# Optimization experiments

Hardware: AMD Instinct MI355X
Metric: run time of the kernel (lower is better)

## Reference

```python
import jax, jax.numpy as jnp
import numpy as np
from jax import lax

B, LS, LT, C, H, GRID = 32, 256, 128, 768, 12, 16
KEEP_RATIO = 0.7

def _ln(x, w, b):
    mu = x.mean(-1, keepdims=True)
    var = ((x - mu) ** 2).mean(-1, keepdims=True)
    return (x - mu) / jnp.sqrt(var + 1e-5) * w + b

def _gelu(x):
    return jax.nn.gelu(x, approximate=False)

def setup_inputs() -> dict:
    key = jax.random.key(0)
    ks = jax.random.split(key, 16)
    w = lambda k, s: jax.random.normal(k, s, jnp.float32) * 0.02
    N = LT + LS
    return {
        'x': jax.random.normal(ks[0], (B, N, C), jnp.float32),
        'global_index_template': jax.random.randint(ks[1], (B, LT), 0, LT).astype(jnp.int32),
        'global_index_search': jax.random.randint(ks[2], (B, LS), 0, LS).astype(jnp.int32),
        'learn_template_mask': jax.random.uniform(ks[3], (2, B, LT // 2), jnp.float32),
        'ln1_w': jnp.ones((C,), jnp.float32), 'ln1_b': jnp.zeros((C,), jnp.float32),
        'qkv_w': w(ks[4], (C, 3 * C)),
        'proj_w': w(ks[5], (C, C)), 'proj_b': jnp.zeros((C,), jnp.float32),
        'ln2_w': jnp.ones((C,), jnp.float32), 'ln2_b': jnp.zeros((C,), jnp.float32),
        'fc1_w': w(ks[6], (C, 4 * C)), 'fc1_b': jnp.zeros((4 * C,), jnp.float32),
        'fc2_w': w(ks[7], (4 * C, C)), 'fc2_b': jnp.zeros((C,), jnp.float32),
        'd1_w': w(ks[8], (3 * C, 768)), 'd1_b': jnp.zeros((768,), jnp.float32),
        'd2_w': w(ks[9], (768, 384)), 'd2_b': jnp.zeros((384,), jnp.float32),
        'd3_w': w(ks[10], (384, 192)), 'd3_b': jnp.zeros((192,), jnp.float32),
        'd4_w': w(ks[11], (192, 1)), 'd4_b': jnp.zeros((1,), jnp.float32),
    }

def reference(x, global_index_template, global_index_search, learn_template_mask,
              ln1_w, ln1_b, qkv_w, proj_w, proj_b, ln2_w, ln2_b,
              fc1_w, fc1_b, fc2_w, fc2_b,
              d1_w, d1_b, d2_w, d2_b, d3_w, d3_b, d4_w, d4_b):
    bs = x.shape[0]
    lt = global_index_template.shape[1]
    ls = global_index_search.shape[1]
    half = lt // 2
    # --- roimax target representations ---
    init_rep = jnp.max(x[:, :half] * learn_template_mask[0][..., None], axis=1, keepdims=True)   # [B,1,C]
    dyn_rep = jnp.max(x[:, half:lt] * learn_template_mask[1][..., None], axis=1, keepdims=True)  # [B,1,C]
    feat = jnp.concatenate([x[:, -ls:],
                            jnp.broadcast_to(init_rep, (bs, ls, C)),
                            jnp.broadcast_to(dyn_rep, (bs, ls, C))], axis=-1)  # [B,ls,3C]
    h = _gelu(feat @ d1_w + d1_b)
    h = _gelu(h @ d2_w + d2_b)
    h = _gelu(h @ d3_w + d3_b)
    pred = h @ d4_w + d4_b                      # [B,ls,1]
    probs = jax.nn.sigmoid(pred)                # foreground probabilities
    # --- 3x3 region-sum conv and argmax center ---
    grid = probs.reshape(bs, 1, GRID, GRID)
    kern = jnp.ones((1, 1, 3, 3), grid.dtype)
    filt = lax.conv_general_dilated(grid, kern, (1, 1), 'SAME',
                                    dimension_numbers=('NCHW', 'OIHW', 'NCHW'))
    max_idx = jnp.argmax(filt.reshape(bs, -1), axis=1)
    cx, cy = max_idx // GRID, max_idx % GRID
    gx = jnp.arange(GRID)[None, :, None]
    gy = jnp.arange(GRID)[None, None, :]
    win = lambda r: ((jnp.abs(gx - cx[:, None, None]) <= r) &
                     (jnp.abs(gy - cy[:, None, None]) <= r)).reshape(bs, GRID * GRID)
    mask7, mask11 = win(3), win(5)
    foreground = (probs > 0.5).astype(jnp.int32)          # [B,ls,1]
    selected_fg = foreground * mask7[..., None].astype(jnp.int32)
    # --- candidate elimination: keep all tokens inside 11x11 window first, then top prob ---
    lens_keep = int(np.ceil(KEEP_RATIO * ls))
    p_out = jnp.where(mask11, jnp.inf, probs[..., 0])     # [B,ls]
    order = jnp.argsort(-p_out, axis=1)                   # stable descending
    topk_idx, non_topk = order[:, :lens_keep], order[:, lens_keep:]
    keep_index = jnp.take_along_axis(global_index_search, topk_idx, axis=1)
    removed_index = jnp.take_along_axis(global_index_search, non_topk, axis=1)
    xs = jnp.take_along_axis(x[:, lt:], topk_idx[..., None], axis=1)  # [B,lens_keep,C]
    xnew = jnp.concatenate([x[:, :lt], xs], axis=1)       # [B, lt+lens_keep, C]
    sf = jnp.take_along_axis(selected_fg, topk_idx[..., None], axis=1)[..., 0]
    decision = jax.nn.one_hot(sf, 2, dtype=x.dtype)       # scatter_(2, sf, 1)
    search_policy = jnp.concatenate([jnp.zeros((bs, lens_keep, 2), x.dtype), decision], -1)
    template_policy = jnp.zeros((bs, half, 4), x.dtype).at[:, :, 0].set(1.0)
    dynamic_policy = jnp.zeros((bs, half, 4), x.dtype).at[:, :, 1].set(1.0)
    P = jnp.concatenate([template_policy, dynamic_policy, search_policy], axis=1)
    key_bg = P[:, :, 2] > 0.5    # background search tokens -> masked as attention keys
    # --- attention ---
    n = xnew.shape[1]
    dh = C // H
    hn = _ln(xnew, ln1_w, ln1_b)
    qkv = (hn @ qkv_w).reshape(bs, n, 3, H, dh).transpose(2, 0, 3, 1, 4)
    q, k, v = qkv[0], qkv[1], qkv[2]
    scores = jnp.einsum('bhnd,bhmd->bhnm', q, k) * dh ** -0.5
    scores = jnp.where(key_bg[:, None, None, :], -1e9, scores)
    attn = jax.nn.softmax(scores, axis=-1)
    out = jnp.einsum('bhnm,bhmd->bhnd', attn, v).transpose(0, 2, 1, 3).reshape(bs, n, C)
    xnew = xnew + (out @ proj_w + proj_b)
    m = _ln(xnew, ln2_w, ln2_b)
    xout = xnew + (_gelu(m @ fc1_w + fc1_b) @ fc2_w + fc2_b)
    return (xout, keep_index, removed_index, attn)
```

## Files before the change

kernel.cpp:

```cpp
#include <hip/hip_runtime.h>
#include <hip/hip_bf16.h>
#include <math.h>

#define BB 32
#define LSN 256
#define LTN 128
#define CCH 768
#define NHH 12
#define NTOK 384
#define NKEEP 180
#define NREM 76
#define NNEW 308
#define MS 8192
#define MN 9856

typedef unsigned short u16;
typedef __attribute__((ext_vector_type(8))) short s8v;
typedef __attribute__((ext_vector_type(4))) float f4v;
typedef __attribute__((ext_vector_type(2))) float f2v;

__device__ __forceinline__ u16 f2bf(float x) {
    union { __hip_bfloat16 b; u16 u; } c; c.b = __float2bfloat16(x); return c.u;
}
__device__ __forceinline__ float bf2f(u16 u) {
    return __uint_as_float(((unsigned)u) << 16);
}
__device__ __forceinline__ void gl_lds16(const u16* g, u16* l) {
    __builtin_amdgcn_global_load_lds((const __attribute__((address_space(1))) unsigned*)g,
                                     (__attribute__((address_space(3))) unsigned*)l, 16, 0, 0);
}
__device__ __forceinline__ int xcd_swz(int lin, int nwg) {
    int q = nwg >> 3, r = nwg & 7;
    int xcd = lin & 7, idx = lin >> 3;
    return (xcd < r ? xcd * (q + 1) : r * (q + 1) + (xcd - r) * q) + idx;
}

__global__ void k_fail(float* o, float v) { o[0] = v; }

__global__ void k_reps(const float* __restrict__ x, const float* __restrict__ mask,
                       float* __restrict__ rep0, float* __restrict__ rep1) {
    int b = blockIdx.x, t = threadIdx.x;
    float m0[3] = {-INFINITY, -INFINITY, -INFINITY};
    float m1[3] = {-INFINITY, -INFINITY, -INFINITY};
    for (int i = 0; i < 64; ++i) {
        float mk0 = mask[b * 64 + i];
        float mk1 = mask[BB * 64 + b * 64 + i];
        const float* r0 = x + (size_t)(b * NTOK + i) * CCH;
        const float* r1 = x + (size_t)(b * NTOK + 64 + i) * CCH;
#pragma unroll
        for (int j = 0; j < 3; ++j) {
            m0[j] = fmaxf(m0[j], r0[t + 256 * j] * mk0);
            m1[j] = fmaxf(m1[j], r1[t + 256 * j] * mk1);
        }
    }
#pragma unroll
    for (int j = 0; j < 3; ++j) {
        rep0[b * CCH + t + 256 * j] = m0[j];
        rep1[b * CCH + t + 256 * j] = m1[j];
    }
}

__device__ __forceinline__ float gelu_np(float v) {
    float t = v / 1.4142135623730951f;
    float ef = (float)erf((double)t);
    return 0.5f * v * (1.0f + ef);
}

template<int ROWMAP>
__global__ __launch_bounds__(256) void gemm_exact(const float* __restrict__ A,
                                                  const float* __restrict__ rep0, const float* __restrict__ rep1,
                                                  const float* __restrict__ W, const float* __restrict__ bias,
                                                  float* __restrict__ out, int N, int K) {
    __shared__ float As[32 * 64];
    __shared__ float Bs[32 * 64];
    int t = threadIdx.x;
    int tx = t & 15, ty = t >> 4;
    int nbx = N >> 6;
    int nwg = nbx * gridDim.y;
    int lin = blockIdx.y * nbx + blockIdx.x;
    int T = xcd_swz(lin, nwg);
    int bxs = T % nbx, bys = T / nbx;
    int bm = bys * 64, bn = bxs * 64;
    int b = bm >> 8;
    f2v acc2[4][2] = {};

    int arow = t >> 2;
    int ak = (t & 3) * 4;
    int asw = arow ^ ((ak & 4) << 2);
    size_t aoff;
    if (ROWMAP) aoff = (size_t)(b * NTOK + LTN + ((bm + arow) & 255)) * CCH;
    else        aoff = (size_t)(bm + arow) * K;

    int bkr = t >> 4, bc = (t & 15) * 4;

#define LOADA(kg) (ROWMAP ? (((kg) < CCH) ? *(const float4*)&A[aoff + (kg)] \
                    : (((kg) < 2*CCH) ? *(const float4*)&rep0[b*CCH + (kg) - CCH] \
                                      : *(const float4*)&rep1[b*CCH + (kg) - 2*CCH])) \
                   : *(const float4*)&A[aoff + (kg)])

    int nt = K >> 5;
    float4 ra0 = LOADA(ak), ra1 = LOADA(16 + ak);
    float4 rb0 = *(const float4*)&W[(size_t)bkr * N + bn + bc];
    float4 rb1 = *(const float4*)&W[(size_t)(16 + bkr) * N + bn + bc];

    for (int tile = 0; tile < nt; ++tile) {
        __syncthreads();
        As[(ak + 0) * 64 + asw] = ra0.x; As[(ak + 1) * 64 + asw] = ra0.y;
        As[(ak + 2) * 64 + asw] = ra0.z; As[(ak + 3) * 64 + asw] = ra0.w;
        As[(16 + ak + 0) * 64 + asw] = ra1.x; As[(16 + ak + 1) * 64 + asw] = ra1.y;
        As[(16 + ak + 2) * 64 + asw] = ra1.z; As[(16 + ak + 3) * 64 + asw] = ra1.w;
        *(float4*)&Bs[t * 4] = rb0;
        *(float4*)&Bs[1024 + t * 4] = rb1;
        if (tile + 1 < nt) {
            int k0 = (tile + 1) << 5;
            ra0 = LOADA(k0 + ak); ra1 = LOADA(k0 + 16 + ak);
            rb0 = *(const float4*)&W[(size_t)(k0 + bkr) * N + bn + bc];
            rb1 = *(const float4*)&W[(size_t)(k0 + 16 + bkr) * N + bn + bc];
        }
        __syncthreads();
#pragma unroll
        for (int k = 0; k < 32; ++k) {
            float a[4], bv[4];
            *(float4*)&a[0]  = *(const float4*)&As[k * 64 + ((ty * 4) ^ ((k & 4) << 2))];
            *(float4*)&bv[0] = *(const float4*)&Bs[k * 64 + tx * 4];
            f2v b0 = {bv[0], bv[1]}, b1 = {bv[2], bv[3]};
#pragma unroll
            for (int i = 0; i < 4; ++i) {
                f2v av = {a[i], a[i]};
                acc2[i][0] = __builtin_elementwise_fma(av, b0, acc2[i][0]);
                acc2[i][1] = __builtin_elementwise_fma(av, b1, acc2[i][1]);
            }
        }
    }
#undef LOADA
#pragma unroll
    for (int i = 0; i < 4; ++i) {
        int m = bm + ty * 4 + i;
        float4 o;
        o.x = gelu_np(acc2[i][0][0] + bias[bn + tx * 4 + 0]);
        o.y = gelu_np(acc2[i][0][1] + bias[bn + tx * 4 + 1]);
        o.z = gelu_np(acc2[i][1][0] + bias[bn + tx * 4 + 2]);
        o.w = gelu_np(acc2[i][1][1] + bias[bn + tx * 4 + 3]);
        *(float4*)&out[(size_t)m * N + bn + tx * 4] = o;
    }
}

__global__ void k_d4sort(const float* __restrict__ h3, const float* __restrict__ w4,
                         const float* __restrict__ b4, const int* __restrict__ gis,
                         float* __restrict__ keep_out, float* __restrict__ rem_out,
                         int* __restrict__ topk, int* __restrict__ keybg) {
    int b = blockIdx.x, t = threadIdx.x;
    __shared__ float pr[256];
    __shared__ double ft[256];
    __shared__ int cxy[2];
    __shared__ float pout[256];
    __shared__ int sf[256];
    __shared__ int ord[256];
    {
        int m = b * 256 + t;
        float acc = 0.f;
        for (int k = 0; k < 192; ++k) acc = fmaf(h3[(size_t)m * 192 + k], w4[k], acc);
        float pred = acc + b4[0];
        float ef = (float)exp(-(double)pred);
        pr[t] = 1.0f / (1.0f + ef);
    }
    __syncthreads();
    int X = t >> 4, Y = t & 15;
    double s = 0.0;
    for (int dx = -1; dx <= 1; ++dx)
        for (int dy = -1; dy <= 1; ++dy) {
            int xx = X + dx, yy = Y + dy;
            if (xx >= 0 && xx < 16 && yy >= 0 && yy < 16) s += (double)pr[xx * 16 + yy];
        }
    ft[t] = s;
    __syncthreads();
    if (t == 0) {
        double best = ft[0]; int bi = 0;
        for (int i = 1; i < 256; ++i) if (ft[i] > best) { best = ft[i]; bi = i; }
        cxy[0] = bi >> 4; cxy[1] = bi & 15;
    }
    __syncthreads();
    int cx = cxy[0], cy = cxy[1];
    int ax = X - cx; if (ax < 0) ax = -ax;
    int ay = Y - cy; if (ay < 0) ay = -ay;
    bool m7  = (ax <= 3) && (ay <= 3);
    bool m11 = (ax <= 5) && (ay <= 5);
    int fg = (pr[t] > 0.5f) ? 1 : 0;
    sf[t] = m7 ? fg : 0;
    pout[t] = m11 ? INFINITY : pr[t];
    __syncthreads();
    float pi = pout[t];
    int rank = 0;
    for (int j = 0; j < 256; ++j) {
        float pj = pout[j];
        rank += (pj > pi) || (pj == pi && j < t);
    }
    ord[rank] = t;
    __syncthreads();
    int idx = ord[t];
    int g = gis[b * 256 + idx];
    if (t < NKEEP) {
        keep_out[b * NKEEP + t] = (float)g;
        topk[b * NKEEP + t] = idx;
        keybg[b * NNEW + LTN + t] = (sf[idx] == 0) ? 1 : 0;
    } else {
        rem_out[b * NREM + (t - NKEEP)] = (float)g;
    }
    if (t < LTN) keybg[b * NNEW + t] = 0;
}

__global__ void k_xnew_ln(const float* __restrict__ x, const int* __restrict__ topk,
                          const float* __restrict__ w, const float* __restrict__ b,
                          float* __restrict__ out_x, u16* __restrict__ hn) {
    int row = blockIdx.x, t = threadIdx.x;
    int bb = row / NNEW, r = row - bb * NNEW;
    int src = (r < LTN) ? r : (LTN + topk[bb * NKEEP + (r - LTN)]);
    const float* p = x + (size_t)(bb * NTOK + src) * CCH;
    __shared__ float s1[256], s2[256];
    float v[3]; float a0 = 0.f, a1 = 0.f;
#pragma unroll
    for (int i = 0; i < 3; ++i) { v[i] = p[t + 256 * i]; a0 += v[i]; a1 += v[i] * v[i]; }
#pragma unroll
    for (int i = 0; i < 3; ++i) out_x[(size_t)row * CCH + t + 256 * i] = v[i];
    s1[t] = a0; s2[t] = a1;
    __syncthreads();
    for (int off = 128; off > 0; off >>= 1) {
        if (t < off) { s1[t] += s1[t + off]; s2[t] += s2[t + off]; }
        __syncthreads();
    }
    float mu = s1[0] * (1.0f / CCH);
    float var = s2[0] * (1.0f / CCH) - mu * mu;
    float rstd = rsqrtf(var + 1e-5f);
#pragma unroll
    for (int i = 0; i < 3; ++i) {
        int c = t + 256 * i;
        hn[(size_t)row * CCH + c] = f2bf((v[i] - mu) * rstd * w[c] + b[c]);
    }
}


__global__ void k_ln_bf(const float* __restrict__ in, const float* __restrict__ w, const float* __restrict__ b,
                        u16* __restrict__ out) {
    int row = blockIdx.x, t = threadIdx.x;
    __shared__ float s1[256], s2[256];
    const float* p = in + (size_t)row * CCH;
    float v[3]; float a0 = 0.f, a1 = 0.f;
#pragma unroll
    for (int i = 0; i < 3; ++i) { v[i] = p[t + 256 * i]; a0 += v[i]; a1 += v[i] * v[i]; }
    s1[t] = a0; s2[t] = a1;
    __syncthreads();
    for (int off = 128; off > 0; off >>= 1) {
        if (t < off) { s1[t] += s1[t + off]; s2[t] += s2[t + off]; }
        __syncthreads();
    }
    float mu = s1[0] * (1.0f / CCH);
    float var = s2[0] * (1.0f / CCH) - mu * mu;
    float rstd = rsqrtf(var + 1e-5f);
#pragma unroll
    for (int i = 0; i < 3; ++i) {
        int c = t + 256 * i;
        out[(size_t)row * CCH + c] = f2bf((v[i] - mu) * rstd * w[c] + b[c]);
    }
}

__global__ void k_prep(const float* __restrict__ qkvw, const float* __restrict__ projw,
                       const float* __restrict__ fc1w, const float* __restrict__ fc2w,
                       u16* __restrict__ qkvwT, u16* __restrict__ projwT,
                       u16* __restrict__ fc1wT, u16* __restrict__ fc2wT) {
    int id = blockIdx.x;
    int t = threadIdx.x;
    const float* W; u16* Wt; int K, N, tile;
    if (id < 1728)      { W = qkvw;  Wt = qkvwT;  K = 768;  N = 2304; tile = id; }
    else if (id < 2304) { W = projw; Wt = projwT; K = 768;  N = 768;  tile = id - 1728; }
    else if (id < 4608) { W = fc1w;  Wt = fc1wT;  K = 768;  N = 3072; tile = id - 2304; }
    else                { W = fc2w;  Wt = fc2wT;  K = 3072; N = 768;  tile = id - 4608; }
    int kt = K >> 5;
    int k0 = (tile % kt) * 32, n0 = (tile / kt) * 32;
    __shared__ float tilebuf[32][33];
    int tx = t & 31, ty = t >> 5;
    for (int i = ty; i < 32; i += 8) tilebuf[i][tx] = W[(size_t)(k0 + i) * N + n0 + tx];
    __syncthreads();
    for (int i = ty; i < 32; i += 8) Wt[(size_t)(n0 + i) * K + k0 + tx] = f2bf(tilebuf[tx][i]);
}

template<int MODE>
__global__ __launch_bounds__(256) void gemm_bf16(const u16* __restrict__ A, const u16* __restrict__ Bt,
                                                 const float* __restrict__ bias, const float* __restrict__ res,
                                                 float* __restrict__ outf, u16* __restrict__ outb,
                                                 u16* __restrict__ vbuf, int N, int K) {
    __shared__ u16 sm[2][2][4096];
    int t = threadIdx.x, lane = t & 63, wid = t >> 6;
    int nwg = gridDim.x * gridDim.y;
    int lin = blockIdx.y * gridDim.x + blockIdx.x;
    int T = xcd_swz(lin, nwg);
    int bx = T % gridDim.x, by = T / gridDim.x;
    int bm = by * 128, bn = bx * 128;
    const u16* pA[2]; const u16* pB[2];
#pragma unroll
    for (int i = 0; i < 2; ++i) {
        int L = wid * 128 + i * 64 + lane;
        int line = L >> 3, sp = L & 7, sl = sp ^ (line & 7);
        int r = (line << 1) | (sl >> 2), k0 = (sl & 3) << 3;
        pA[i] = A + (size_t)(bm + r) * K + k0;
        pB[i] = Bt + (size_t)(bn + r) * K + k0;
    }
    int wr = wid >> 1, wc = wid & 1;
    int l15 = lane & 15, l4 = lane >> 4;
    int rA = wr * 64 + l15, rB = wc * 64 + l15;
    int offA = (rA >> 1) * 128 + (((((rA & 1) << 2) | l4)) ^ ((rA >> 1) & 7)) * 16;
    int offB = (rB >> 1) * 128 + (((((rB & 1) << 2) | l4)) ^ ((rB >> 1) & 7)) * 16;
    f4v zero = {0.f, 0.f, 0.f, 0.f};
    f4v acc[4][4];
#pragma unroll
    for (int i = 0; i < 4; ++i)
#pragma unroll
        for (int j = 0; j < 4; ++j) acc[i][j] = zero;

#define STAGE_G(buf, kt) { \
    u16* da = &sm[buf][0][wid * 1024]; u16* db = &sm[buf][1][wid * 1024]; \
    gl_lds16(pA[0] + (kt) * 32, da); \
    gl_lds16(pA[1] + (kt) * 32, da + 512); \
    gl_lds16(pB[0] + (kt) * 32, db); \
    gl_lds16(pB[1] + (kt) * 32, db + 512); \
}
    int nk = K >> 5;
    STAGE_G(0, 0);
    __syncthreads();
    for (int kt = 0; kt < nk; ++kt) {
        int cur = kt & 1;
        if (kt + 1 < nk) STAGE_G(cur ^ 1, kt + 1);
        const char* bA = (const char*)&sm[cur][0][0];
        const char* bBp = (const char*)&sm[cur][1][0];
        s8v a[4], b[4];
#pragma unroll
        for (int i = 0; i < 4; ++i) {
            a[i] = *(const s8v*)(bA + offA + i * 1024);
            b[i] = *(const s8v*)(bBp + offB + i * 1024);
        }
#pragma unroll
        for (int mf = 0; mf < 4; ++mf)
#pragma unroll
            for (int nf = 0; nf < 4; ++nf)
                acc[mf][nf] = __builtin_amdgcn_mfma_f32_16x16x32_bf16(a[mf], b[nf], acc[mf][nf], 0, 0, 0);
        __syncthreads();
    }
#undef STAGE_G
#pragma unroll
    for (int mf = 0; mf < 4; ++mf)
#pragma unroll
        for (int nf = 0; nf < 4; ++nf)
#pragma unroll
            for (int j = 0; j < 4; ++j) {
                int row = bm + wr * 64 + mf * 16 + l4 * 4 + j;
                int col = bn + wc * 64 + nf * 16 + l15;
                float v = acc[mf][nf][j];
                if (MODE == 0) {
                    if (col < 1536) {
                        if (col < 768) v *= 0.125f;
                        outb[(size_t)row * 1536 + col] = f2bf(v);
                    } else {
                        vbuf[(size_t)row * 768 + (col - 1536)] = f2bf(v);
                    }
                } else if (MODE == 1) {
                    outf[(size_t)row * N + col] = v + bias[col] + res[(size_t)row * N + col];
                } else {
                    float g = v + bias[col];
                    g = 0.5f * g * (1.0f + erff(g * 0.70710678f));
                    outb[(size_t)row * N + col] = f2bf(g);
                }
            }
}

__global__ __launch_bounds__(256) void k_attn2(const u16* __restrict__ qkvQK, const u16* __restrict__ vbuf,
                                               const int* __restrict__ keybg,
                                               float* __restrict__ attn_out, u16* __restrict__ ctx) {
    __shared__ __align__(16) char smem[98560];
    u16* Qs = (u16*)smem;
    u16* Ks = (u16*)(smem + 9216);
    u16* Ss = (u16*)(smem + 55296);
    int* kb = (int*)(smem + 97280);
    float* OT = (float*)Ss;
    u16* Vts = Ks;

    int nwg = gridDim.x * gridDim.y;
    int lin = blockIdx.y * gridDim.x + blockIdx.x;
    int T = xcd_swz(lin, nwg);
    int bh = T / 5;
    int q0 = (T - bh * 5) * 64;
    int b = bh / NHH, h = bh % NHH;
    int nq = NNEW - q0; if (nq > 64) nq = 64;
    int t = threadIdx.x, lane = t & 63, wid = t >> 6;
    int l15 = lane & 15, l4 = lane >> 4;
    s8v z = {0, 0, 0, 0, 0, 0, 0, 0};

    {
        int r = t >> 2, c = (t & 3) * 16;
        u16* dst = Qs + r * 72 + c;
        if (r < nq) {
            const u16* src = qkvQK + (size_t)(b * NNEW + q0 + r) * 1536 + h * 64 + c;
            *(s8v*)dst = *(const s8v*)src;
            *(s8v*)(dst + 8) = *(const s8v*)(src + 8);
        } else { *(s8v*)dst = z; *(s8v*)(dst + 8) = z; }
    }
    for (int it = 0; it < 5; ++it) {
        int r = it * 64 + (t >> 2), c = (t & 3) * 16;
        u16* dst = Ks + r * 72 + c;
        if (r < NNEW) {
            const u16* src = qkvQK + (size_t)(b * NNEW + r) * 1536 + 768 + h * 64 + c;
            *(s8v*)dst = *(const s8v*)src;
            *(s8v*)(dst + 8) = *(const s8v*)(src + 8);
        } else { *(s8v*)dst = z; *(s8v*)(dst + 8) = z; }
    }
    for (int i = t; i < 320; i += 256) kb[i] = (i < NNEW) ? keybg[b * NNEW + i] : 1;
    __syncthreads();

    f4v zero = {0.f, 0.f, 0.f, 0.f};
    f4v acc[4][5];
#pragma unroll
    for (int i = 0; i < 4; ++i)
#pragma unroll
        for (int j = 0; j < 5; ++j) acc[i][j] = zero;
#pragma unroll
    for (int ks = 0; ks < 2; ++ks) {
        s8v a[4], bf[5];
#pragma unroll
        for (int mf = 0; mf < 4; ++mf) a[mf] = *(const s8v*)(Qs + (mf * 16 + l15) * 72 + ks * 32 + l4 * 8);
#pragma unroll
        for (int nf = 0; nf < 5; ++nf) bf[nf] = *(const s8v*)(Ks + (wid * 80 + nf * 16 + l15) * 72 + ks * 32 + l4 * 8);
#pragma unroll
        for (int mf = 0; mf < 4; ++mf)
#pragma unroll
            for (int nf = 0; nf < 5; ++nf)
                acc[mf][nf] = __builtin_amdgcn_mfma_f32_16x16x32_bf16(a[mf], bf[nf], acc[mf][nf], 0, 0, 0);
    }
#pragma unroll
    for (int nf = 0; nf < 5; ++nf) {
        int n = wid * 80 + nf * 16 + l15;
        int msk = kb[n];
#pragma unroll
        for (int mf = 0; mf < 4; ++mf)
#pragma unroll
            for (int j = 0; j < 4; ++j) {
                int q = mf * 16 + l4 * 4 + j;
                float v = msk ? -1e9f : acc[mf][nf][j];
                Ss[q * 328 + n] = f2bf(v);
            }
    }
    __syncthreads();

    {
        for (int it = 0; it < 5; ++it) {
            int tok = it * 64 + (t >> 2);
            int d0 = (t & 3) * 16;
            if (tok < NNEW) {
                const u16* src = vbuf + (size_t)(b * NNEW + tok) * 768 + h * 64 + d0;
                s8v v0 = *(const s8v*)src;
                s8v v1 = *(const s8v*)(src + 8);
#pragma unroll
                for (int j = 0; j < 8; ++j) Vts[(d0 + j) * 328 + tok] = (u16)v0[j];
#pragma unroll
                for (int j = 0; j < 8; ++j) Vts[(d0 + 8 + j) * 328 + tok] = (u16)v1[j];
            } else if (tok < 320) {
#pragma unroll
                for (int j = 0; j < 16; ++j) Vts[(d0 + j) * 328 + tok] = 0;
            }
        }
    }
    {
        int q = t >> 2, j4 = t & 3;
        u16* row = Ss + q * 328 + j4 * 80;
        float mx = -3e38f;
#pragma unroll
        for (int i = 0; i < 10; ++i) {
            s8v vv = *(const s8v*)(row + i * 8);
#pragma unroll
            for (int e = 0; e < 8; ++e) mx = fmaxf(mx, bf2f((u16)vv[e]));
        }
        mx = fmaxf(mx, __shfl_xor(mx, 1));
        mx = fmaxf(mx, __shfl_xor(mx, 2));
        float sum = 0.f;
#pragma unroll
        for (int i = 0; i < 10; ++i) {
            s8v vv = *(const s8v*)(row + i * 8);
            s8v ov;
#pragma unroll
            for (int e = 0; e < 8; ++e) {
                float ex = expf(bf2f((u16)vv[e]) - mx);
                sum += ex;
                ov[e] = (short)f2bf(ex);
            }
            *(s8v*)(row + i * 8) = ov;
        }
        sum += __shfl_xor(sum, 1);
        sum += __shfl_xor(sum, 2);
        float inv = 1.0f / sum;
#pragma unroll
        for (int i = 0; i < 10; ++i) {
            s8v vv = *(const s8v*)(row + i * 8);
            s8v ov;
            float pf[8];
#pragma unroll
            for (int e = 0; e < 8; ++e) {
                float p = bf2f((u16)vv[e]) * inv;
                pf[e] = p;
                ov[e] = (short)f2bf(p);
            }
            *(s8v*)(row + i * 8) = ov;
            if (q < nq) {
                int n0 = j4 * 80 + i * 8;
                float* dst = attn_out + ((size_t)bh * NNEW + q0 + q) * NNEW + n0;
#pragma unroll
                for (int e = 0; e < 8; ++e) if (n0 + e < NNEW) dst[e] = pf[e];
            }
        }
    }
    __syncthreads();

    f4v o[4];
#pragma unroll
    for (int i = 0; i < 4; ++i) o[i] = zero;
    int dblk = wid * 16;
#pragma unroll
    for (int ks = 0; ks < 10; ++ks) {
        s8v av = *(const s8v*)(Vts + (dblk + l15) * 328 + ks * 32 + l4 * 8);
#pragma unroll
        for (int nf = 0; nf < 4; ++nf) {
            s8v pv = *(const s8v*)(Ss + (nf * 16 + l15) * 328 + ks * 32 + l4 * 8);
            o[nf] = __builtin_amdgcn_mfma_f32_16x16x32_bf16(av, pv, o[nf], 0, 0, 0);
        }
    }
    __syncthreads();
#pragma unroll
    for (int nf = 0; nf < 4; ++nf)
#pragma unroll
        for (int j = 0; j < 4; ++j)
            OT[(dblk + l4 * 4 + j) * 65 + nf * 16 + l15] = o[nf][j];
    __syncthreads();
    {
        int q = t >> 2, c = t & 3;
        if (q < nq) {
            u16 buf[16];
#pragma unroll
            for (int i = 0; i < 16; ++i) buf[i] = f2bf(OT[(c * 16 + i) * 65 + q]);
            u16* dst = ctx + (size_t)(b * NNEW + q0 + q) * CCH + h * 64 + c * 16;
            *(s8v*)dst = *(const s8v*)&buf[0];
            *(s8v*)(dst + 8) = *(const s8v*)&buf[8];
        }
    }
}

extern "C" void kernel_launch(void* const* d_in, const int* in_sizes, int n_in,
                              void* d_out, int out_size, void* d_ws, size_t ws_size,
                              hipStream_t stream) {
    const float* x     = (const float*)d_in[0];
    const int*   gis   = (const int*)d_in[2];
    const float* mask  = (const float*)d_in[3];
    const float* ln1w  = (const float*)d_in[4];
    const float* ln1b  = (const float*)d_in[5];
    const float* qkvw  = (const float*)d_in[6];
    const float* projw = (const float*)d_in[7];
    const float* projb = (const float*)d_in[8];
    const float* ln2w  = (const float*)d_in[9];
    const float* ln2b  = (const float*)d_in[10];
    const float* fc1w  = (const float*)d_in[11];
    const float* fc1b  = (const float*)d_in[12];
    const float* fc2w  = (const float*)d_in[13];
    const float* fc2b  = (const float*)d_in[14];
    const float* d1w   = (const float*)d_in[15];
    const float* d1b   = (const float*)d_in[16];
    const float* d2w   = (const float*)d_in[17];
    const float* d2b   = (const float*)d_in[18];
    const float* d3w   = (const float*)d_in[19];
    const float* d3b   = (const float*)d_in[20];
    const float* d4w   = (const float*)d_in[21];
    const float* d4b   = (const float*)d_in[22];

    float* out_x    = (float*)d_out;
    float* out_keep = out_x + 7569408;
    float* out_rem  = out_keep + 5760;
    float* out_attn = out_rem + 2432;

    char* ws = (char*)d_ws;
    u16* hn_bf  = (u16*)(ws);
    u16* qkvQK  = (u16*)(ws + 15138816);
    u16* vbuf   = (u16*)(ws + 45416448);
    u16* fc1_bf = (u16*)(ws);
    u16* ctx_bf = (u16*)(ws + 60751872);
    u16* qkvwT  = (u16*)(ws + 75890688);
    u16* projwT = (u16*)(ws + 79429632);
    u16* fc1wT  = (u16*)(ws + 80609280);
    u16* fc2wT  = (u16*)(ws + 85327872);
    char* misc  = ws + 90046464;
    float* rep0  = (float*)(misc + 0 * 262144);
    float* rep1  = (float*)(misc + 1 * 262144);
    int*   topk  = (int*)(misc + 5 * 262144);
    int*   keybg = (int*)(misc + 6 * 262144);
    size_t required = 90046464ull + 7ull * 262144ull;
    if (ws_size < required) {
        k_fail<<<1, 1, 0, stream>>>((float*)d_out, (float)(ws_size / 1048576.0));
        return;
    }

    float* h1 = (float*)out_attn;
    float* h2 = h1 + 8192 * 768;
    float* h3 = h2 + 8192 * 384;

    k_prep<<<6912, 256, 0, stream>>>(qkvw, projw, fc1w, fc2w, qkvwT, projwT, fc1wT, fc2wT);

    k_reps<<<BB, 256, 0, stream>>>(x, mask, rep0, rep1);
    gemm_exact<1><<<dim3(12, 128), 256, 0, stream>>>(x, rep0, rep1, d1w, d1b, h1, 768, 2304);
    gemm_exact<0><<<dim3(6, 128), 256, 0, stream>>>(h1, nullptr, nullptr, d2w, d2b, h2, 384, 768);
    gemm_exact<0><<<dim3(3, 128), 256, 0, stream>>>(h2, nullptr, nullptr, d3w, d3b, h3, 192, 384);
    k_d4sort<<<BB, 256, 0, stream>>>(h3, d4w, d4b, gis, out_keep, out_rem, topk, keybg);
    k_xnew_ln<<<MN, 256, 0, stream>>>(x, topk, ln1w, ln1b, out_x, hn_bf);

    gemm_bf16<0><<<dim3(18, 77), 256, 0, stream>>>(hn_bf, qkvwT, nullptr, nullptr, nullptr, qkvQK, vbuf, 2304, 768);
    k_attn2<<<dim3(5, 384), 256, 0, stream>>>(qkvQK, vbuf, keybg, out_attn, ctx_bf);
    gemm_bf16<1><<<dim3(6, 77), 256, 0, stream>>>(ctx_bf, projwT, projb, out_x, out_x, nullptr, nullptr, 768, 768);
    k_ln_bf<<<MN, 256, 0, stream>>>(out_x, ln2w, ln2b, ctx_bf);
    gemm_bf16<2><<<dim3(24, 77), 256, 0, stream>>>(ctx_bf, fc1wT, fc1b, nullptr, nullptr, fc1_bf, nullptr, 3072, 768);
    gemm_bf16<1><<<dim3(6, 77), 256, 0, stream>>>(fc1_bf, fc2wT, fc2b, out_x, out_x, nullptr, nullptr, 768, 3072);
}
```

Measured before the change: 991.1 us.

## Fuse d1 GEMM with weight prep, smaller d3 tiles, vectorize LayerNorms, MFMA priority

The weight transpose/convert kernel is merged into the d1 GEMM launch as extra blocks, so the memory-bound prep runs alongside the compute-bound GEMM and one launch is removed. The d3 GEMM switches to 32-row tiles to double its block count for better occupancy. Both LayerNorm kernels now use float4 loads and stores with 192 active threads. s_setprio is raised around the MFMA loops in attention. The merged kernel shares one LDS size and register budget across both roles, which may limit occupancy.

```diff
diff --git a/kernel.cpp b/kernel.cpp
--- a/kernel.cpp
+++ b/kernel.cpp
@@ -18,6 +18,7 @@
 typedef __attribute__((ext_vector_type(8))) short s8v;
 typedef __attribute__((ext_vector_type(4))) float f4v;
 typedef __attribute__((ext_vector_type(2))) float f2v;
+typedef __attribute__((ext_vector_type(4))) unsigned short u4v;
 
 __device__ __forceinline__ u16 f2bf(float x) {
     union { __hip_bfloat16 b; u16 u; } c; c.b = __float2bfloat16(x); return c.u;
@@ -64,6 +65,109 @@
     float t = v / 1.4142135623730951f;
     float ef = (float)erf((double)t);
     return 0.5f * v * (1.0f + ef);
+}
+
+__device__ __forceinline__ void d1_body(const float* __restrict__ A,
+                                        const float* __restrict__ rep0, const float* __restrict__ rep1,
+                                        const float* __restrict__ W, const float* __restrict__ bias,
+                                        float* __restrict__ out, float* As, float* Bs, int lin) {
+    const int N = 768, K = 2304;
+    int t = threadIdx.x;
+    int tx = t & 15, ty = t >> 4;
+    int T = xcd_swz(lin, 1536);
+    int bxs = T % 12, bys = T / 12;
+    int bm = bys * 64, bn = bxs * 64;
+    int b = bm >> 8;
+    f2v acc2[4][2] = {};
+
+    int arow = t >> 2;
+    int ak = (t & 3) * 4;
+    int asw = arow ^ ((ak & 4) << 2);
+    size_t aoff = (size_t)(b * NTOK + LTN + ((bm + arow) & 255)) * CCH;
+
+    int bkr = t >> 4, bc = (t & 15) * 4;
+
+#define LOADA1(kg) ((((kg) < CCH) ? *(const float4*)&A[aoff + (kg)] \
+                    : (((kg) < 2*CCH) ? *(const float4*)&rep0[b*CCH + (kg) - CCH] \
+                                      : *(const float4*)&rep1[b*CCH + (kg) - 2*CCH])))
+    int nt = K >> 5;
+    float4 ra0 = LOADA1(ak), ra1 = LOADA1(16 + ak);
+    float4 rb0 = *(const float4*)&W[(size_t)bkr * N + bn + bc];
+    float4 rb1 = *(const float4*)&W[(size_t)(16 + bkr) * N + bn + bc];
+
+    for (int tile = 0; tile < nt; ++tile) {
+        __syncthreads();
+        As[(ak + 0) * 64 + asw] = ra0.x; As[(ak + 1) * 64 + asw] = ra0.y;
+        As[(ak + 2) * 64 + asw] = ra0.z; As[(ak + 3) * 64 + asw] = ra0.w;
+        As[(16 + ak + 0) * 64 + asw] = ra1.x; As[(16 + ak + 1) * 64 + asw] = ra1.y;
+        As[(16 + ak + 2) * 64 + asw] = ra1.z; As[(16 + ak + 3) * 64 + asw] = ra1.w;
+        *(float4*)&Bs[t * 4] = rb0;
+        *(float4*)&Bs[1024 + t * 4] = rb1;
+        if (tile + 1 < nt) {
+            int k0 = (tile + 1) << 5;
+            ra0 = LOADA1(k0 + ak); ra1 = LOADA1(k0 + 16 + ak);
+            rb0 = *(const float4*)&W[(size_t)(k0 + bkr) * N + bn + bc];
+            rb1 = *(const float4*)&W[(size_t)(k0 + 16 + bkr) * N + bn + bc];
+        }
+        __syncthreads();
+#pragma unroll
+        for (int k = 0; k < 32; ++k) {
+            float a[4], bv[4];
+            *(float4*)&a[0]  = *(const float4*)&As[k * 64 + ((ty * 4) ^ ((k & 4) << 2))];
+            *(float4*)&bv[0] = *(const float4*)&Bs[k * 64 + tx * 4];
+            f2v b0 = {bv[0], bv[1]}, b1 = {bv[2], bv[3]};
+#pragma unroll
+            for (int i = 0; i < 4; ++i) {
+                f2v av = {a[i], a[i]};
+                acc2[i][0] = __builtin_elementwise_fma(av, b0, acc2[i][0]);
+                acc2[i][1] = __builtin_elementwise_fma(av, b1, acc2[i][1]);
+            }
+        }
+    }
+#undef LOADA1
+#pragma unroll
+    for (int i = 0; i < 4; ++i) {
+        int m = bm + ty * 4 + i;
+        float4 o;
+        o.x = gelu_np(acc2[i][0][0] + bias[bn + tx * 4 + 0]);
+        o.y = gelu_np(acc2[i][0][1] + bias[bn + tx * 4 + 1]);
+        o.z = gelu_np(acc2[i][1][0] + bias[bn + tx * 4 + 2]);
+        o.w = gelu_np(acc2[i][1][1] + bias[bn + tx * 4 + 3]);
+        *(float4*)&out[(size_t)m * N + bn + tx * 4] = o;
+    }
+}
+
+__device__ __forceinline__ void prep_body(const float* __restrict__ qkvw, const float* __restrict__ projw,
+                                          const float* __restrict__ fc1w, const float* __restrict__ fc2w,
+                                          u16* __restrict__ qkvwT, u16* __restrict__ projwT,
+                                          u16* __restrict__ fc1wT, u16* __restrict__ fc2wT,
+                                          float* tilebuf, int id) {
+    int t = threadIdx.x;
+    const float* W; u16* Wt; int K, N, tile;
+    if (id < 1728)      { W = qkvw;  Wt = qkvwT;  K = 768;  N = 2304; tile = id; }
+    else if (id < 2304) { W = projw; Wt = projwT; K = 768;  N = 768;  tile = id - 1728; }
+    else if (id < 4608) { W = fc1w;  Wt = fc1wT;  K = 768;  N = 3072; tile = id - 2304; }
+    else                { W = fc2w;  Wt = fc2wT;  K = 3072; N = 768;  tile = id - 4608; }
+    int kt = K >> 5;
+    int k0 = (tile % kt) * 32, n0 = (tile / kt) * 32;
+    int tx = t & 31, ty = t >> 5;
+    for (int i = ty; i < 32; i += 8) tilebuf[i * 33 + tx] = W[(size_t)(k0 + i) * N + n0 + tx];
+    __syncthreads();
+    for (int i = ty; i < 32; i += 8) Wt[(size_t)(n0 + i) * K + k0 + tx] = f2bf(tilebuf[tx * 33 + i]);
+}
+
+__global__ __launch_bounds__(256) void k_d1prep(const float* __restrict__ x,
+                                                const float* __restrict__ rep0, const float* __restrict__ rep1,
+                                                const float* __restrict__ d1w, const float* __restrict__ d1b,
+                                                float* __restrict__ h1,
+                                                const float* __restrict__ qkvw, const float* __restrict__ projw,
+                                                const float* __restrict__ fc1w, const float* __restrict__ fc2w,
+                                                u16* __restrict__ qkvwT, u16* __restrict__ projwT,
+                                                u16* __restrict__ fc1wT, u16* __restrict__ fc2wT) {
+    __shared__ __align__(16) float smem[4096];
+    int id = blockIdx.x;
+    if (id < 1536) d1_body(x, rep0, rep1, d1w, d1b, h1, smem, smem + 2048, id);
+    else           prep_body(qkvw, projw, fc1w, fc2w, qkvwT, projwT, fc1wT, fc2wT, smem, id - 1536);
 }
 
 template<int ROWMAP>
@@ -136,6 +240,70 @@
 #pragma unroll
     for (int i = 0; i < 4; ++i) {
         int m = bm + ty * 4 + i;
+        float4 o;
+        o.x = gelu_np(acc2[i][0][0] + bias[bn + tx * 4 + 0]);
+        o.y = gelu_np(acc2[i][0][1] + bias[bn + tx * 4 + 1]);
+        o.z = gelu_np(acc2[i][1][0] + bias[bn + tx * 4 + 2]);
+        o.w = gelu_np(acc2[i][1][1] + bias[bn + tx * 4 + 3]);
+        *(float4*)&out[(size_t)m * N + bn + tx * 4] = o;
+    }
+}
+
+__global__ __launch_bounds__(256) void gemm_exact32(const float* __restrict__ A,
+                                                    const float* __restrict__ W, const float* __restrict__ bias,
+                                                    float* __restrict__ out, int N, int K) {
+    __shared__ float As[32 * 33];
+    __shared__ float Bs[32 * 64];
+    int t = threadIdx.x;
+    int tx = t & 15, ty = t >> 4;
+    int nbx = N >> 6;
+    int nwg = nbx * gridDim.y;
+    int lin = blockIdx.y * nbx + blockIdx.x;
+    int T = xcd_swz(lin, nwg);
+    int bxs = T % nbx, bys = T / nbx;
+    int bm = bys * 32, bn = bxs * 64;
+    f2v acc2[2][2] = {};
+
+    int arow = t >> 3;
+    int ak = (t & 7) * 4;
+    size_t aoff = (size_t)(bm + arow) * K;
+    int bkr = t >> 4, bc = (t & 15) * 4;
+
+    int nt = K >> 5;
+    float4 ra = *(const float4*)&A[aoff + ak];
+    float4 rb0 = *(const float4*)&W[(size_t)bkr * N + bn + bc];
+    float4 rb1 = *(const float4*)&W[(size_t)(16 + bkr) * N + bn + bc];
+
+    for (int tile = 0; tile < nt; ++tile) {
+        __syncthreads();
+        As[(ak + 0) * 33 + arow] = ra.x; As[(ak + 1) * 33 + arow] = ra.y;
+        As[(ak + 2) * 33 + arow] = ra.z; As[(ak + 3) * 33 + arow] = ra.w;
+        *(float4*)&Bs[t * 4] = rb0;
+        *(float4*)&Bs[1024 + t * 4] = rb1;
+        if (tile + 1 < nt) {
+            int k0 = (tile + 1) << 5;
+            ra = *(const float4*)&A[aoff + k0 + ak];
+            rb0 = *(const float4*)&W[(size_t)(k0 + bkr) * N + bn + bc];
+            rb1 = *(const float4*)&W[(size_t)(k0 + 16 + bkr) * N + bn + bc];
+        }
+        __syncthreads();
+#pragma unroll
+        for (int k = 0; k < 32; ++k) {
+            float a0 = As[k * 33 + ty * 2];
+            float a1 = As[k * 33 + ty * 2 + 1];
+            float bv[4];
+            *(float4*)&bv[0] = *(const float4*)&Bs[k * 64 + tx * 4];
+            f2v b0 = {bv[0], bv[1]}, b1 = {bv[2], bv[3]};
+            f2v av0 = {a0, a0}, av1 = {a1, a1};
+            acc2[0][0] = __builtin_elementwise_fma(av0, b0, acc2[0][0]);
+            acc2[0][1] = __builtin_elementwise_fma(av0, b1, acc2[0][1]);
+            acc2[1][0] = __builtin_elementwise_fma(av1, b0, acc2[1][0]);
+            acc2[1][1] = __builtin_elementwise_fma(av1, b1, acc2[1][1]);
+        }
+    }
+#pragma unroll
+    for (int i = 0; i < 2; ++i) {
+        int m = bm + ty * 2 + i;
         float4 o;
         o.x = gelu_np(acc2[i][0][0] + bias[bn + tx * 4 + 0]);
         o.y = gelu_np(acc2[i][0][1] + bias[bn + tx * 4 + 1]);
@@ -217,11 +385,14 @@
     int src = (r < LTN) ? r : (LTN + topk[bb * NKEEP + (r - LTN)]);
     const float* p = x + (size_t)(bb * NTOK + src) * CCH;
     __shared__ float s1[256], s2[256];
-    float v[3]; float a0 = 0.f, a1 = 0.f;
-#pragma unroll
-    for (int i = 0; i < 3; ++i) { v[i] = p[t + 256 * i]; a0 += v[i]; a1 += v[i] * v[i]; }
-#pragma unroll
-    for (int i = 0; i < 3; ++i) out_x[(size_t)row * CCH + t + 256 * i] = v[i];
+    float4 v = {0.f, 0.f, 0.f, 0.f};
+    float a0 = 0.f, a1 = 0.f;
+    if (t < 192) {
+        v = *(const float4*)&p[t * 4];
+        a0 = v.x + v.y + v.z + v.w;
+        a1 = v.x * v.x + v.y * v.y + v.z * v.z + v.w * v.w;
+        *(float4*)&out_x[(size_t)row * CCH + t * 4] = v;
+    }
     s1[t] = a0; s2[t] = a1;
     __syncthreads();
     for (int off = 128; off > 0; off >>= 1) {
@@ -231,22 +402,30 @@
     float mu = s1[0] * (1.0f / CCH);
     float var = s2[0] * (1.0f / CCH) - mu * mu;
     float rstd = rsqrtf(var + 1e-5f);
-#pragma unroll
-    for (int i = 0; i < 3; ++i) {
-        int c = t + 256 * i;
-        hn[(size_t)row * CCH + c] = f2bf((v[i] - mu) * rstd * w[c] + b[c]);
-    }
-}
-
+    if (t < 192) {
+        float4 wv = *(const float4*)&w[t * 4];
+        float4 bv = *(const float4*)&b[t * 4];
+        u4v o;
+        o[0] = f2bf((v.x - mu) * rstd * wv.x + bv.x);
+        o[1] = f2bf((v.y - mu) * rstd * wv.y + bv.y);
+        o[2] = f2bf((v.z - mu) * rstd * wv.z + bv.z);
+        o[3] = f2bf((v.w - mu) * rstd * wv.w + bv.w);
+        *(u4v*)&hn[(size_t)row * CCH + t * 4] = o;
+    }
+}
 
 __global__ void k_ln_bf(const float* __restrict__ in, const float* __restrict__ w, const float* __restrict__ b,
                         u16* __restrict__ out) {
     int row = blockIdx.x, t = threadIdx.x;
     __shared__ float s1[256], s2[256];
     const float* p = in + (size_t)row * CCH;
-    float v[3]; float a0 = 0.f, a1 = 0.f;
-#pragma unroll
-    for (int i = 0; i < 3; ++i) { v[i] = p[t + 256 * i]; a0 += v[i]; a1 += v[i] * v[i]; }
+    float4 v = {0.f, 0.f, 0.f, 0.f};
+    float a0 = 0.f, a1 = 0.f;
+    if (t < 192) {
+        v = *(const float4*)&p[t * 4];
+        a0 = v.x + v.y + v.z + v.w;
+        a1 = v.x * v.x + v.y * v.y + v.z * v.z + v.w * v.w;
+    }
     s1[t] = a0; s2[t] = a1;
     __syncthreads();
     for (int off = 128; off > 0; off >>= 1) {
@@ -256,31 +435,16 @@
     float mu = s1[0] * (1.0f / CCH);
     float var = s2[0] * (1.0f / CCH) - mu * mu;
     float rstd = rsqrtf(var + 1e-5f);
-#pragma unroll
-    for (int i = 0; i < 3; ++i) {
-        int c = t + 256 * i;
-        out[(size_t)row * CCH + c] = f2bf((v[i] - mu) * rstd * w[c] + b[c]);
-    }
-}
-
-__global__ void k_prep(const float* __restrict__ qkvw, const float* __restrict__ projw,
-                       const float* __restrict__ fc1w, const float* __restrict__ fc2w,
-                       u16* __restrict__ qkvwT, u16* __restrict__ projwT,
-                       u16* __restrict__ fc1wT, u16* __restrict__ fc2wT) {
-    int id = blockIdx.x;
-    int t = threadIdx.x;
-    const float* W; u16* Wt; int K, N, tile;
-    if (id < 1728)      { W = qkvw;  Wt = qkvwT;  K = 768;  N = 2304; tile = id; }
-    else if (id < 2304) { W = projw; Wt = projwT; K = 768;  N = 768;  tile = id - 1728; }
-    else if (id < 4608) { W = fc1w;  Wt = fc1wT;  K = 768;  N = 3072; tile = id - 2304; }
-    else                { W = fc2w;  Wt = fc2wT;  K = 3072; N = 768;  tile = id - 4608; }
-    int kt = K >> 5;
-    int k0 = (tile % kt) * 32, n0 = (tile / kt) * 32;
-    __shared__ float tilebuf[32][33];
-    int tx = t & 31, ty = t >> 5;
-    for (int i = ty; i < 32; i += 8) tilebuf[i][tx] = W[(size_t)(k0 + i) * N + n0 + tx];
-    __syncthreads();
-    for (int i = ty; i < 32; i += 8) Wt[(size_t)(n0 + i) * K + k0 + tx] = f2bf(tilebuf[tx][i]);
+    if (t < 192) {
+        float4 wv = *(const float4*)&w[t * 4];
+        float4 bv = *(const float4*)&b[t * 4];
+        u4v o;
+        o[0] = f2bf((v.x - mu) * rstd * wv.x + bv.x);
+        o[1] = f2bf((v.y - mu) * rstd * wv.y + bv.y);
+        o[2] = f2bf((v.z - mu) * rstd * wv.z + bv.z);
+        o[3] = f2bf((v.w - mu) * rstd * wv.w + bv.w);
+        *(u4v*)&out[(size_t)row * CCH + t * 4] = o;
+    }
 }
 
 template<int MODE>
@@ -420,6 +584,7 @@
     for (int i = 0; i < 4; ++i)
 #pragma unroll
         for (int j = 0; j < 5; ++j) acc[i][j] = zero;
+    __builtin_amdgcn_s_setprio(1);
 #pragma unroll
     for (int ks = 0; ks < 2; ++ks) {
         s8v a[4], bf[5];
@@ -433,6 +598,7 @@
             for (int nf = 0; nf < 5; ++nf)
                 acc[mf][nf] = __builtin_amdgcn_mfma_f32_16x16x32_bf16(a[mf], bf[nf], acc[mf][nf], 0, 0, 0);
     }
+    __builtin_amdgcn_s_setprio(0);
 #pragma unroll
     for (int nf = 0; nf < 5; ++nf) {
         int n = wid * 80 + nf * 16 + l15;
@@ -520,6 +686,7 @@
 #pragma unroll
     for (int i = 0; i < 4; ++i) o[i] = zero;
     int dblk = wid * 16;
+    __builtin_amdgcn_s_setprio(1);
 #pragma unroll
     for (int ks = 0; ks < 10; ++ks) {
         s8v av = *(const s8v*)(Vts + (dblk + l15) * 328 + ks * 32 + l4 * 8);
@@ -529,6 +696,7 @@
             o[nf] = __builtin_amdgcn_mfma_f32_16x16x32_bf16(av, pv, o[nf], 0, 0, 0);
         }
     }
+    __builtin_amdgcn_s_setprio(0);
     __syncthreads();
 #pragma unroll
     for (int nf = 0; nf < 4; ++nf)
@@ -605,12 +773,11 @@
     float* h2 = h1 + 8192 * 768;
     float* h3 = h2 + 8192 * 384;
 
-    k_prep<<<6912, 256, 0, stream>>>(qkvw, projw, fc1w, fc2w, qkvwT, projwT, fc1wT, fc2wT);
-
     k_reps<<<BB, 256, 0, stream>>>(x, mask, rep0, rep1);
-    gemm_exact<1><<<dim3(12, 128), 256, 0, stream>>>(x, rep0, rep1, d1w, d1b, h1, 768, 2304);
+    k_d1prep<<<8448, 256, 0, stream>>>(x, rep0, rep1, d1w, d1b, h1,
+                                       qkvw, projw, fc1w, fc2w, qkvwT, projwT, fc1wT, fc2wT);
     gemm_exact<0><<<dim3(6, 128), 256, 0, stream>>>(h1, nullptr, nullptr, d2w, d2b, h2, 384, 768);
-    gemm_exact<0><<<dim3(3, 128), 256, 0, stream>>>(h2, nullptr, nullptr, d3w, d3b, h3, 192, 384);
+    gemm_exact32<<<dim3(3, 256), 256, 0, stream>>>(h2, d3w, d3b, h3, 192, 384);
     k_d4sort<<<BB, 256, 0, stream>>>(h3, d4w, d4b, gis, out_keep, out_rem, topk, keybg);
     k_xnew_ln<<<MN, 256, 0, stream>>>(x, topk, ln1w, ln1b, out_x, hn_bf);
 
```

After: 1.300 ms (median of 4 runs). 1.31x slower.
